# Kernel optimization log

Hardware: AMD Instinct MI355X
Metric: run time of the kernel (lower is better)

Reference implementation:

```python
import jax, jax.numpy as jnp
import numpy as np
import math

B, N, T, H, HEADS, FIN, NL_TR = 4, 256, 16, 128, 4, 2, 5
M = B * N
NEG = -1e9

def _sinusoidal(t, h):
    pos = jnp.arange(t, dtype=jnp.float32)[:, None]
    div = jnp.exp(jnp.arange(0, h, 2, dtype=jnp.float32) * (-math.log(10000.0) / h))
    pe = jnp.zeros((t, h), dtype=jnp.float32)
    pe = pe.at[:, 0::2].set(jnp.sin(pos * div))
    pe = pe.at[:, 1::2].set(jnp.cos(pos * div))
    return pe

def _gat(x, W, a_src, a_dst, b, E, m):
    # x: [T,M,F]; W: [F,heads,H]; E: [T,M,M] bool, E[t,i,j]=edge j->i; m: [T,M] bool
    h = jnp.einsum('tmf,fhd->tmhd', x, W)
    ss = jnp.einsum('tmhd,hd->tmh', h, a_src)  # source score per node
    sd = jnp.einsum('tmhd,hd->tmh', h, a_dst)  # dest score per node
    logits = jax.nn.leaky_relu(sd[:, :, None, :] + ss[:, None, :, :], 0.2)  # [T,i,j,h]
    logits = jnp.where(E[..., None], logits, NEG)
    alpha = jax.nn.softmax(logits, axis=2)  # segment-softmax over incoming edges
    out = jnp.einsum('tijh,tjhd->tihd', alpha, h).mean(axis=2) + b  # concat=False -> head mean + bias
    return jax.nn.relu(out) * m[..., None]

def _ln(x, s, b):
    mu = x.mean(-1, keepdims=True)
    v = ((x - mu) ** 2).mean(-1, keepdims=True)
    return (x - mu) / jnp.sqrt(v + 1e-5) * s + b

def _forward(ego_mask, positions, adjacency, gat1_W, gat1_asrc, gat1_adst, gat1_b, gatW, gat_asrc, gat_adst, gat_b, Wqkv, bqkv, Wo, bo, ln1_s, ln1_b, ln2_s, ln2_b, Wff1, bff1, Wff2, bff2):
    m = jnp.transpose(ego_mask, (1, 0, 2)).reshape(T, M)  # [T, B*N]
    eye = jnp.eye(M, dtype=bool)
    # edge j->i valid iff A[t,j,i]!=0 and both nodes masked; PyG GATConv adds self-loops
    E = ((jnp.swapaxes(adjacency, 1, 2) != 0) & m[:, :, None] & m[:, None, :]) | (eye[None] & m[:, :, None])
    x = _gat(positions, gat1_W, gat1_asrc, gat1_adst, gat1_b, E, m)
    for i in range(5):
        x = _gat(x, gatW[i], gat_asrc[i], gat_adst[i], gat_b[i], E, m)
    x_seq = jnp.transpose(x, (1, 0, 2)) + _sinusoidal(T, H)[None]  # [M, T, H]
    dh = H // HEADS
    scale = 1.0 / math.sqrt(dh)
    for l in range(NL_TR):
        q = (x_seq @ Wqkv[l, 0] + bqkv[l, 0]).reshape(M, T, HEADS, dh)
        k = (x_seq @ Wqkv[l, 1] + bqkv[l, 1]).reshape(M, T, HEADS, dh)
        v = (x_seq @ Wqkv[l, 2] + bqkv[l, 2]).reshape(M, T, HEADS, dh)
        sc = jnp.einsum('bqhd,bkhd->bhqk', q, k) * scale
        a = jax.nn.softmax(sc, axis=-1)
        o = jnp.einsum('bhqk,bkhd->bqhd', a, v).reshape(M, T, H) @ Wo[l] + bo[l]
        x_seq = _ln(x_seq + o, ln1_s[l], ln1_b[l])
        f = jax.nn.relu(x_seq @ Wff1[l] + bff1[l]) @ Wff2[l] + bff2[l]
        x_seq = _ln(x_seq + f, ln2_s[l], ln2_b[l])
    return x_seq.reshape(B, N, T, H)

def setup_inputs() -> dict:
    key = jax.random.key(0)
    ks = jax.random.split(key, 32)
    s = 0.05
    f32 = jnp.float32
    inp = {
        'ego_mask': jax.random.uniform(ks[0], (B, T, N)) < 0.95,
        'positions': jax.random.normal(ks[1], (T, M, FIN), dtype=f32),
        'adjacency': (jax.random.uniform(ks[2], (T, M, M)) < 0.02).astype(f32),
        'gat1_W': jax.random.normal(ks[3], (FIN, HEADS, H), dtype=f32) * s,
        'gat1_asrc': jax.random.normal(ks[4], (HEADS, H), dtype=f32) * s,
        'gat1_adst': jax.random.normal(ks[5], (HEADS, H), dtype=f32) * s,
        'gat1_b': jnp.zeros((H,), dtype=f32),
        'gatW': jax.random.normal(ks[6], (5, H, HEADS, H), dtype=f32) * s,
        'gat_asrc': jax.random.normal(ks[7], (5, HEADS, H), dtype=f32) * s,
        'gat_adst': jax.random.normal(ks[8], (5, HEADS, H), dtype=f32) * s,
        'gat_b': jnp.zeros((5, H), dtype=f32),
        'Wqkv': jax.random.normal(ks[9], (NL_TR, 3, H, H), dtype=f32) * s,
        'bqkv': jnp.zeros((NL_TR, 3, H), dtype=f32),
        'Wo': jax.random.normal(ks[10], (NL_TR, H, H), dtype=f32) * s,
        'bo': jnp.zeros((NL_TR, H), dtype=f32),
        'ln1_s': jnp.ones((NL_TR, H), dtype=f32),
        'ln1_b': jnp.zeros((NL_TR, H), dtype=f32),
        'ln2_s': jnp.ones((NL_TR, H), dtype=f32),
        'ln2_b': jnp.zeros((NL_TR, H), dtype=f32),
        'Wff1': jax.random.normal(ks[11], (NL_TR, H, 4 * H), dtype=f32) * s,
        'bff1': jnp.zeros((NL_TR, 4 * H), dtype=f32),
        'Wff2': jax.random.normal(ks[12], (NL_TR, 4 * H, H), dtype=f32) * s,
        'bff2': jnp.zeros((NL_TR, H), dtype=f32),
    }
    return inp

def reference(ego_mask, positions, adjacency, gat1_W, gat1_asrc, gat1_adst, gat1_b, gatW, gat_asrc, gat_adst, gat_b, Wqkv, bqkv, Wo, bo, ln1_s, ln1_b, ln2_s, ln2_b, Wff1, bff1, Wff2, bff2):
    return _forward(ego_mask, positions, adjacency, gat1_W, gat1_asrc, gat1_adst, gat1_b, gatW, gat_asrc, gat_adst, gat_b, Wqkv, bqkv, Wo, bo, ln1_s, ln1_b, ln2_s, ln2_b, Wff1, bff1, Wff2, bff2)
```

## Files before the change

### kernel.cpp

```cpp
#include <hip/hip_runtime.h>
#include <hip/hip_bf16.h>

#define TT 16
#define MM 1024
#define HDIM 128
#define NHEADS 4
#define NROWS (TT*MM)
#define MAXDEG 64

typedef __bf16 bf16x8 __attribute__((ext_vector_type(8)));
typedef float f32x4 __attribute__((ext_vector_type(4)));

__device__ __forceinline__ unsigned short f2b(float x) {
    unsigned u = __float_as_uint(x);
    u += 0x7fff + ((u >> 16) & 1);
    return (unsigned short)(u >> 16);
}
__device__ __forceinline__ float bu2f(unsigned short u) {
    return __uint_as_float(((unsigned)u) << 16);
}

__global__ __launch_bounds__(256) void k_init(const int* __restrict__ ego,
                                              float* __restrict__ mfl,
                                              int* __restrict__ cnt) {
    int idx = blockIdx.x * 256 + threadIdx.x;
    int t = idx >> 10, i = idx & 1023;
    int b = i >> 8, n = i & 255;
    mfl[idx] = ego[b * (TT * 256) + t * 256 + n] ? 1.f : 0.f;
    cnt[idx] = 0;
}

__global__ __launch_bounds__(256) void k_edges(const float* __restrict__ adj,
                                               const float* __restrict__ mfl,
                                               int* __restrict__ cnt,
                                               int* __restrict__ nbr) {
    int bid = blockIdx.x;
    int t = bid >> 6, jc = bid & 63;
    int tid = threadIdx.x;
    int i0 = tid * 4;
    int rowb = t * MM;
    float mi[4];
#pragma unroll
    for (int r = 0; r < 4; ++r) mi[r] = mfl[rowb + i0 + r];
    __shared__ float ms[16];
    if (tid < 16) ms[tid] = mfl[rowb + jc * 16 + tid];
    __syncthreads();
    const float* at = adj + (size_t)t * MM * MM;
#pragma unroll 4
    for (int jj = 0; jj < 16; ++jj) {
        int j = jc * 16 + jj;
        float4 a = *(const float4*)(at + (size_t)j * MM + i0);
        float mj = ms[jj];
#pragma unroll
        for (int r = 0; r < 4; ++r) {
            int i = i0 + r;
            bool e;
            if (j == i) e = (mi[r] != 0.f);
            else e = ((&a.x)[r] != 0.f) && (mj != 0.f) && (mi[r] != 0.f);
            if (e) {
                int row = rowb + i;
                int pos = atomicAdd(&cnt[row], 1);
                if (pos < MAXDEG) nbr[(size_t)row * MAXDEG + pos] = j;
            }
        }
    }
}

__global__ __launch_bounds__(256) void k_prep(const float* __restrict__ Wqkv,
                                              const float* __restrict__ Wo,
                                              const float* __restrict__ Wff1,
                                              const float* __restrict__ Wff2,
                                              const float* __restrict__ gW,
                                              unsigned short* __restrict__ Wb) {
    int o = blockIdx.x * 256 + threadIdx.x;
    const float* src; int cs;
    if (o < 122880) {
        int l = o / 24576, r = o % 24576;
        if (r < 6144) {
            int nt = r >> 8, rem = r & 255, ks = rem >> 6, lane = rem & 63;
            int mt = nt >> 3, cc = nt & 7;
            int k = ks * 32 + ((lane >> 4) << 3), c = cc * 16 + (lane & 15);
            src = Wqkv + ((size_t)(l * 3 + mt) * 128 + k) * 128 + c; cs = 128;
        } else if (r < 8192) {
            int u = r - 6144, nt = u >> 8, rem = u & 255, ks = rem >> 6, lane = rem & 63;
            int k = ks * 32 + ((lane >> 4) << 3), c = nt * 16 + (lane & 15);
            src = Wo + (size_t)l * 16384 + (size_t)k * 128 + c; cs = 128;
        } else if (r < 16384) {
            int u = r - 8192, nt = u >> 8, rem = u & 255, ks = rem >> 6, lane = rem & 63;
            int k = ks * 32 + ((lane >> 4) << 3), c = nt * 16 + (lane & 15);
            src = Wff1 + (size_t)l * 65536 + (size_t)k * 512 + c; cs = 512;
        } else {
            int u = r - 16384, nt = u >> 10, rem = u & 1023, ks = rem >> 6, lane = rem & 63;
            int k = ks * 32 + ((lane >> 4) << 3), c = nt * 16 + (lane & 15);
            src = Wff2 + (size_t)l * 65536 + (size_t)k * 128 + c; cs = 128;
        }
    } else {
        int u = o - 122880;
        int l = u >> 13, rr = u & 8191;
        int nt = rr >> 8, rem = rr & 255, ks = rem >> 6, lane = rem & 63;
        int k = ks * 32 + ((lane >> 4) << 3), c = nt * 16 + (lane & 15);
        src = gW + (size_t)l * 65536 + (size_t)k * 512 + c; cs = 512;
    }
    unsigned v[4];
#pragma unroll
    for (int j = 0; j < 4; ++j)
        v[j] = (unsigned)f2b(src[(2 * j) * (size_t)cs]) |
               ((unsigned)f2b(src[(2 * j + 1) * (size_t)cs]) << 16);
    *(uint4*)(Wb + (size_t)o * 8) = make_uint4(v[0], v[1], v[2], v[3]);
}

__global__ __launch_bounds__(128) void k_gat1(const float* __restrict__ x,
                                              const float* __restrict__ W,
                                              const float* __restrict__ asrc,
                                              const float* __restrict__ adst,
                                              unsigned short* __restrict__ h16,
                                              float* __restrict__ ss,
                                              float* __restrict__ sd) {
    int bid = blockIdx.x;
    int row = ((bid & 7) << 11) + (bid >> 3);
    int tid = threadIdx.x;
    float x0 = x[row * 2], x1 = x[row * 2 + 1];
    float s4[4], d4[4];
#pragma unroll
    for (int hh = 0; hh < 4; ++hh) {
        int o = hh * 128 + tid;
        float v = x0 * W[o] + x1 * W[512 + o];
        h16[(size_t)row * 512 + o] = f2b(v);
        s4[hh] = v * asrc[o];
        d4[hh] = v * adst[o];
    }
#pragma unroll
    for (int hh = 0; hh < 4; ++hh)
        for (int off = 32; off; off >>= 1) {
            s4[hh] += __shfl_down(s4[hh], off, 64);
            d4[hh] += __shfl_down(d4[hh], off, 64);
        }
    __shared__ float red[2][2][4];
    if ((tid & 63) == 0) {
        int w = tid >> 6;
#pragma unroll
        for (int hh = 0; hh < 4; ++hh) { red[w][0][hh] = s4[hh]; red[w][1][hh] = d4[hh]; }
    }
    __syncthreads();
    if (tid < 4) ss[row * 4 + tid] = red[0][0][tid] + red[1][0][tid];
    else if (tid < 8) sd[row * 4 + tid - 4] = red[0][1][tid - 4] + red[1][1][tid - 4];
}

__global__ __launch_bounds__(256, 2) void k_gat_h(const unsigned short* __restrict__ x16,
                                                  const unsigned short* __restrict__ Wg,
                                                  const float* __restrict__ asrc,
                                                  const float* __restrict__ adst,
                                                  unsigned short* __restrict__ h16,
                                                  float* __restrict__ ss,
                                                  float* __restrict__ sd) {
    __shared__ __align__(16) unsigned short xb[32 * 136];
    int bid = blockIdx.x;
    int row0 = (((bid & 7) << 6) + (bid >> 3)) * 32;
    int tid = threadIdx.x;
#pragma unroll
    for (int q = 0; q < 2; ++q) {
        int u = tid + q * 256;
        int rr = u >> 4, cc = (u & 15) * 8;
        *(uint4*)(xb + rr * 136 + cc) = *(const uint4*)(x16 + (size_t)(row0 + rr) * 128 + cc);
    }
    __syncthreads();
    const int lane = tid & 63, w = tid >> 6;
    const int mrow = lane & 15, quad = lane >> 4;
    float ps[2][4] = {{0,0,0,0},{0,0,0,0}}, pd[2][4] = {{0,0,0,0},{0,0,0,0}};
#pragma unroll
    for (int ib = 0; ib < 4; ++ib) {
        bf16x8 wb[8];
#pragma unroll
        for (int u = 0; u < 2; ++u) {
            int nt = w * 8 + ib * 2 + u;
#pragma unroll
            for (int ks = 0; ks < 4; ++ks)
                wb[u * 4 + ks] = *(const bf16x8*)(Wg + (size_t)((nt * 4 + ks) * 64 + lane) * 8);
        }
#pragma unroll
        for (int rg = 0; rg < 2; ++rg) {
            bf16x8 af[4];
#pragma unroll
            for (int ks = 0; ks < 4; ++ks)
                af[ks] = *(const bf16x8*)(xb + (rg * 16 + mrow) * 136 + ks * 32 + quad * 8);
            f32x4 acc[2];
            acc[0] = (f32x4){0.f, 0.f, 0.f, 0.f};
            acc[1] = (f32x4){0.f, 0.f, 0.f, 0.f};
#pragma unroll
            for (int u = 0; u < 2; ++u)
#pragma unroll
                for (int ks = 0; ks < 4; ++ks)
                    acc[u] = __builtin_amdgcn_mfma_f32_16x16x32_bf16(af[ks], wb[u * 4 + ks], acc[u], 0, 0, 0);
#pragma unroll
            for (int u = 0; u < 2; ++u) {
                int nt = w * 8 + ib * 2 + u, col = nt * 16 + mrow;
                float as_ = asrc[col], ad_ = adst[col];
#pragma unroll
                for (int r = 0; r < 4; ++r) {
                    float v = acc[u][r];
                    h16[(size_t)(row0 + rg * 16 + quad * 4 + r) * 512 + col] = f2b(v);
                    ps[rg][r] += v * as_; pd[rg][r] += v * ad_;
                }
            }
        }
    }
#pragma unroll
    for (int off = 1; off < 16; off <<= 1)
#pragma unroll
        for (int rg = 0; rg < 2; ++rg)
#pragma unroll
            for (int r = 0; r < 4; ++r) {
                ps[rg][r] += __shfl_xor(ps[rg][r], off, 64);
                pd[rg][r] += __shfl_xor(pd[rg][r], off, 64);
            }
    if (mrow == 0) {
#pragma unroll
        for (int rg = 0; rg < 2; ++rg)
#pragma unroll
            for (int r = 0; r < 4; ++r) {
                int row = row0 + rg * 16 + quad * 4 + r;
                ss[row * 4 + w] = ps[rg][r];
                sd[row * 4 + w] = pd[rg][r];
            }
    }
}

__global__ __launch_bounds__(256, 2) void k_agg(const unsigned short* __restrict__ h16,
                                                const float* __restrict__ ss,
                                                const float* __restrict__ sd,
                                                const int* __restrict__ cnt,
                                                const int* __restrict__ nbr,
                                                const float* __restrict__ mfl,
                                                const float* __restrict__ bias,
                                                unsigned short* __restrict__ xo16) {
    __shared__ float alB[4][MAXDEG][4];
    __shared__ int   nbB[4][MAXDEG];
    __shared__ __align__(16) float partB[4][512];
    int bid = blockIdx.x;
    int row0 = (((bid & 7) << 9) + (bid >> 3)) * 4;
    int tid = threadIdx.x;
    const int w = tid >> 6, lane = tid & 63;
    int row = row0 + w, t = row >> 10;
    bool valid = mfl[row] != 0.f;
    int c = 0;
    if (valid) { c = cnt[row]; if (c > MAXDEG) c = MAXDEG; }
    bool act = lane < c;
    int jreg = 0;
    float lg[4];
    if (act) {
        jreg = nbr[(size_t)row * MAXDEG + lane];
        int jr = t * MM + jreg;
#pragma unroll
        for (int hh = 0; hh < 4; ++hh) {
            float v = sd[row * 4 + hh] + ss[jr * 4 + hh];
            lg[hh] = v > 0.f ? v : 0.2f * v;
        }
    } else {
#pragma unroll
        for (int hh = 0; hh < 4; ++hh) lg[hh] = -1e30f;
    }
    float mx[4];
#pragma unroll
    for (int hh = 0; hh < 4; ++hh) mx[hh] = lg[hh];
#pragma unroll
    for (int off = 32; off; off >>= 1)
#pragma unroll
        for (int hh = 0; hh < 4; ++hh) mx[hh] = fmaxf(mx[hh], __shfl_xor(mx[hh], off, 64));
    float ev[4];
#pragma unroll
    for (int hh = 0; hh < 4; ++hh) ev[hh] = act ? __expf(lg[hh] - mx[hh]) : 0.f;
    float sm[4];
#pragma unroll
    for (int hh = 0; hh < 4; ++hh) sm[hh] = ev[hh];
#pragma unroll
    for (int off = 32; off; off >>= 1)
#pragma unroll
        for (int hh = 0; hh < 4; ++hh) sm[hh] += __shfl_xor(sm[hh], off, 64);
    if (act) {
        float4 a4 = make_float4(ev[0] / sm[0], ev[1] / sm[1], ev[2] / sm[2], ev[3] / sm[3]);
        *(float4*)&alB[w][lane][0] = a4;
        nbB[w][lane] = jreg;
    }
    __syncthreads();
    const int head = lane >> 4;
    float acc[8] = {0, 0, 0, 0, 0, 0, 0, 0};
    const unsigned short* hb = h16 + (size_t)t * MM * 512 + lane * 8;
    for (int n = 0; n < c; ++n) {
        int j = nbB[w][n];
        float a = alB[w][n][head];
        uint4 v = *(const uint4*)(hb + (size_t)j * 512);
        acc[0] += a * bu2f((unsigned short)(v.x & 0xffff));
        acc[1] += a * bu2f((unsigned short)(v.x >> 16));
        acc[2] += a * bu2f((unsigned short)(v.y & 0xffff));
        acc[3] += a * bu2f((unsigned short)(v.y >> 16));
        acc[4] += a * bu2f((unsigned short)(v.z & 0xffff));
        acc[5] += a * bu2f((unsigned short)(v.z >> 16));
        acc[6] += a * bu2f((unsigned short)(v.w & 0xffff));
        acc[7] += a * bu2f((unsigned short)(v.w >> 16));
    }
    *(float4*)&partB[w][lane * 8]     = make_float4(acc[0], acc[1], acc[2], acc[3]);
    *(float4*)&partB[w][lane * 8 + 4] = make_float4(acc[4], acc[5], acc[6], acc[7]);
    __syncthreads();
    {
        int d0 = lane * 2;
        unsigned outp = 0;
#pragma unroll
        for (int q = 0; q < 2; ++q) {
            int d = d0 + q;
            float v = 0.f;
            if (valid) {
                v = 0.25f * (partB[w][d] + partB[w][128 + d] + partB[w][256 + d] + partB[w][384 + d])
                    + bias[d];
                v = fmaxf(v, 0.f);
            }
            outp |= ((unsigned)f2b(v)) << (16 * q);
        }
        *(unsigned*)(xo16 + (size_t)row * 128 + d0) = outp;
    }
}

__device__ __forceinline__ void ln512(float* xs, unsigned short* xbB,
                                      const float* s, const float* b) {
    int tid = threadIdx.x, row = tid >> 4, lane = tid & 15;
    float* xr = xs + row * 128;
    float sum = 0.f;
#pragma unroll
    for (int k2 = 0; k2 < 8; ++k2) sum += xr[lane + 16 * k2];
#pragma unroll
    for (int off = 8; off; off >>= 1) sum += __shfl_xor(sum, off, 16);
    float mean = sum * (1.f / 128.f);
    float vs = 0.f;
#pragma unroll
    for (int k2 = 0; k2 < 8; ++k2) { float d = xr[lane + 16 * k2] - mean; vs += d * d; }
#pragma unroll
    for (int off = 8; off; off >>= 1) vs += __shfl_xor(vs, off, 16);
    float rstd = rsqrtf(vs * (1.f / 128.f) + 1e-5f);
#pragma unroll
    for (int k2 = 0; k2 < 8; ++k2) {
        int d = lane + 16 * k2;
        float v = (xr[d] - mean) * rstd * s[d] + b[d];
        xr[d] = v;
        xbB[row * 136 + d] = f2b(v);
    }
    __syncthreads();
}

__global__ __launch_bounds__(512, 2) void k_tf(const unsigned short* __restrict__ xg,
        const unsigned short* __restrict__ Wb,
        const float* __restrict__ bqkv, const float* __restrict__ bo,
        const float* __restrict__ ln1s, const float* __restrict__ ln1b,
        const float* __restrict__ ln2s, const float* __restrict__ ln2b,
        const float* __restrict__ bff1, const float* __restrict__ bff2,
        float* __restrict__ out) {
    __shared__ __align__(16) float smem[16640];
    float* xs  = smem;
    float* sbB = smem + 4096;
    unsigned short* xbB  = (unsigned short*)(smem + 6144);
    unsigned short* qkvB = (unsigned short*)(smem + 8320);
    const int m0 = blockIdx.x * 2, tid = threadIdx.x;
    const int lane = tid & 63, w = tid >> 6;
    const int sid = w >> 2, w4 = w & 3;
    const int mrow = lane & 15, quad = lane >> 4;
    unsigned short* xb16  = xbB + sid * 2176;
    unsigned short* Qb16  = qkvB + sid * 8320;
    unsigned short* Kb16  = Qb16 + 2176;
    unsigned short* Vb16  = Qb16 + 4352;
    unsigned short* hid16 = Qb16;
    float* sb  = sbB + sid * 1024;
    float* xss = xs + sid * 2048;

    for (int idx = tid; idx < 4096; idx += 512) {
        int sq = idx >> 11, t = (idx >> 7) & 15, d = idx & 127, jj = d >> 1;
        float arg = (float)t * expf(-(float)(2 * jj) * (9.210340371976184f / 128.f));
        float pe = (d & 1) ? cosf(arg) : sinf(arg);
        xs[idx] = bu2f(xg[(size_t)t * (MM * HDIM) + (size_t)(m0 + sq) * HDIM + d]) + pe;
    }
    __syncthreads();
    {
        const int crow = tid >> 4, ccb = (tid & 15) * 8;
        const float* xp = xs + crow * 128 + ccb;
        unsigned v[4];
#pragma unroll
        for (int j = 0; j < 4; ++j)
            v[j] = (unsigned)f2b(xp[2 * j]) | ((unsigned)f2b(xp[2 * j + 1]) << 16);
        *(uint4*)(xbB + crow * 136 + ccb) = make_uint4(v[0], v[1], v[2], v[3]);
    }
    __syncthreads();

    for (int l = 0; l < 5; ++l) {
        const unsigned short* Wl = Wb + (size_t)l * 196608;
        {
            bf16x8 af[4];
#pragma unroll
            for (int ks = 0; ks < 4; ++ks)
                af[ks] = *(const bf16x8*)(xb16 + mrow * 136 + ks * 32 + quad * 8);
#pragma unroll
            for (int ib = 0; ib < 3; ++ib) {
                bf16x8 wb[8];
#pragma unroll
                for (int u = 0; u < 2; ++u) {
                    int nt = w4 * 6 + ib * 2 + u;
                    const unsigned short* bp = Wl + (size_t)(nt * 4) * 512 + lane * 8;
#pragma unroll
                    for (int ks = 0; ks < 4; ++ks)
                        wb[u * 4 + ks] = *(const bf16x8*)(bp + ks * 512);
                }
                f32x4 acc[2];
                acc[0] = (f32x4){0.f, 0.f, 0.f, 0.f};
                acc[1] = (f32x4){0.f, 0.f, 0.f, 0.f};
#pragma unroll
                for (int u = 0; u < 2; ++u)
#pragma unroll
                    for (int ks = 0; ks < 4; ++ks)
                        acc[u] = __builtin_amdgcn_mfma_f32_16x16x32_bf16(af[ks], wb[u * 4 + ks], acc[u], 0, 0, 0);
#pragma unroll
                for (int u = 0; u < 2; ++u) {
                    int nt = w4 * 6 + ib * 2 + u, mt = nt >> 3, cc = nt & 7;
                    int col = cc * 16 + mrow;
                    float bb = bqkv[l * 384 + mt * 128 + col];
                    unsigned short* dst = (mt == 0) ? Qb16 : (mt == 1) ? Kb16 : Vb16;
#pragma unroll
                    for (int r = 0; r < 4; ++r)
                        dst[(quad * 4 + r) * 136 + col] = f2b(acc[u][r] + bb);
                }
            }
        }
        __syncthreads();
        {
            int hh = w4, tq = (tid >> 2) & 15, tk0 = (tid & 3) * 4;
            const unsigned short* qp = Qb16 + tq * 136 + hh * 32;
            float a[4] = {0.f, 0.f, 0.f, 0.f};
#pragma unroll
            for (int d4 = 0; d4 < 4; ++d4) {
                uint4 qv = *(const uint4*)(qp + d4 * 8);
                float qf[8];
                qf[0] = bu2f((unsigned short)(qv.x & 0xffff)); qf[1] = bu2f((unsigned short)(qv.x >> 16));
                qf[2] = bu2f((unsigned short)(qv.y & 0xffff)); qf[3] = bu2f((unsigned short)(qv.y >> 16));
                qf[4] = bu2f((unsigned short)(qv.z & 0xffff)); qf[5] = bu2f((unsigned short)(qv.z >> 16));
                qf[6] = bu2f((unsigned short)(qv.w & 0xffff)); qf[7] = bu2f((unsigned short)(qv.w >> 16));
#pragma unroll
                for (int j = 0; j < 4; ++j) {
                    uint4 kv = *(const uint4*)(Kb16 + (tk0 + j) * 136 + hh * 32 + d4 * 8);
                    a[j] += qf[0] * bu2f((unsigned short)(kv.x & 0xffff));
                    a[j] += qf[1] * bu2f((unsigned short)(kv.x >> 16));
                    a[j] += qf[2] * bu2f((unsigned short)(kv.y & 0xffff));
                    a[j] += qf[3] * bu2f((unsigned short)(kv.y >> 16));
                    a[j] += qf[4] * bu2f((unsigned short)(kv.z & 0xffff));
                    a[j] += qf[5] * bu2f((unsigned short)(kv.z >> 16));
                    a[j] += qf[6] * bu2f((unsigned short)(kv.w & 0xffff));
                    a[j] += qf[7] * bu2f((unsigned short)(kv.w >> 16));
                }
            }
#pragma unroll
            for (int j = 0; j < 4; ++j)
                sb[(tk0 + j) * 64 + hh * 16 + tq] = a[j] * 0.17677669529663687f;
        }
        __syncthreads();
        if (tid < 128) {
            float* sbp = sbB + (tid >> 6) * 1024;
            int cc = tid & 63;
            float mx = -1e30f;
#pragma unroll
            for (int u = 0; u < 16; ++u) mx = fmaxf(mx, sbp[u * 64 + cc]);
            float s = 0.f;
#pragma unroll
            for (int u = 0; u < 16; ++u) { float e = __expf(sbp[u * 64 + cc] - mx); sbp[u * 64 + cc] = e; s += e; }
            float inv = 1.f / s;
#pragma unroll
            for (int u = 0; u < 16; ++u) sbp[u * 64 + cc] *= inv;
        }
        __syncthreads();
        {
            int o = tid & 127, r0p = ((tid >> 7) & 1) * 8, hh = o >> 5;
            float accp[8] = {0, 0, 0, 0, 0, 0, 0, 0};
            for (int u = 0; u < 16; ++u) {
                float vv = bu2f(Vb16[u * 136 + o]);
                const float* pp = sb + u * 64 + hh * 16 + r0p;
#pragma unroll
                for (int r = 0; r < 8; ++r) accp[r] += pp[r] * vv;
            }
#pragma unroll
            for (int r = 0; r < 8; ++r)
                xb16[(r0p + r) * 136 + o] = f2b(accp[r]);
        }
        __syncthreads();
        {
            bf16x8 af[4];
#pragma unroll
            for (int ks = 0; ks < 4; ++ks)
                af[ks] = *(const bf16x8*)(xb16 + mrow * 136 + ks * 32 + quad * 8);
            const unsigned short* Ws = Wl + 49152;
            bf16x8 wb[8];
#pragma unroll
            for (int u = 0; u < 2; ++u) {
                int nt = w4 * 2 + u;
#pragma unroll
                for (int ks = 0; ks < 4; ++ks)
                    wb[u * 4 + ks] = *(const bf16x8*)(Ws + (size_t)((nt * 4 + ks) * 64 + lane) * 8);
            }
            f32x4 acc[2];
            acc[0] = (f32x4){0.f, 0.f, 0.f, 0.f};
            acc[1] = (f32x4){0.f, 0.f, 0.f, 0.f};
#pragma unroll
            for (int u = 0; u < 2; ++u)
#pragma unroll
                for (int ks = 0; ks < 4; ++ks)
                    acc[u] = __builtin_amdgcn_mfma_f32_16x16x32_bf16(af[ks], wb[u * 4 + ks], acc[u], 0, 0, 0);
#pragma unroll
            for (int u = 0; u < 2; ++u) {
                int col = (w4 * 2 + u) * 16 + mrow;
                float bb = bo[l * 128 + col];
#pragma unroll
                for (int r = 0; r < 4; ++r)
                    xss[(quad * 4 + r) * 128 + col] += acc[u][r] + bb;
            }
        }
        __syncthreads();
        ln512(xs, xbB, ln1s + l * 128, ln1b + l * 128);
        {
            bf16x8 af[4];
#pragma unroll
            for (int ks = 0; ks < 4; ++ks)
                af[ks] = *(const bf16x8*)(xb16 + mrow * 136 + ks * 32 + quad * 8);
            const unsigned short* Ws = Wl + 65536;
#pragma unroll
            for (int ib = 0; ib < 4; ++ib) {
                bf16x8 wb[8];
#pragma unroll
                for (int u = 0; u < 2; ++u) {
                    int nt = w4 * 8 + ib * 2 + u;
#pragma unroll
                    for (int ks = 0; ks < 4; ++ks)
                        wb[u * 4 + ks] = *(const bf16x8*)(Ws + (size_t)((nt * 4 + ks) * 64 + lane) * 8);
                }
                f32x4 acc[2];
                acc[0] = (f32x4){0.f, 0.f, 0.f, 0.f};
                acc[1] = (f32x4){0.f, 0.f, 0.f, 0.f};
#pragma unroll
                for (int u = 0; u < 2; ++u)
#pragma unroll
                    for (int ks = 0; ks < 4; ++ks)
                        acc[u] = __builtin_amdgcn_mfma_f32_16x16x32_bf16(af[ks], wb[u * 4 + ks], acc[u], 0, 0, 0);
#pragma unroll
                for (int u = 0; u < 2; ++u) {
                    int col = (w4 * 8 + ib * 2 + u) * 16 + mrow;
                    float bb = bff1[l * 512 + col];
#pragma unroll
                    for (int r = 0; r < 4; ++r) {
                        float v = fmaxf(acc[u][r] + bb, 0.f);
                        hid16[(quad * 4 + r) * 520 + col] = f2b(v);
                    }
                }
            }
        }
        __syncthreads();
        {
            f32x4 a0 = (f32x4){0.f, 0.f, 0.f, 0.f};
            f32x4 a1 = (f32x4){0.f, 0.f, 0.f, 0.f};
            const unsigned short* Ws = Wl + 131072;
            int nt0 = w4 * 2, nt1 = w4 * 2 + 1;
#pragma unroll
            for (int kb = 0; kb < 4; ++kb) {
                bf16x8 afb[4], w0[4], w1[4];
#pragma unroll
                for (int kk = 0; kk < 4; ++kk) {
                    int ks = kb * 4 + kk;
                    afb[kk] = *(const bf16x8*)(hid16 + mrow * 520 + ks * 32 + quad * 8);
                    w0[kk] = *(const bf16x8*)(Ws + (size_t)((nt0 * 16 + ks) * 64 + lane) * 8);
                    w1[kk] = *(const bf16x8*)(Ws + (size_t)((nt1 * 16 + ks) * 64 + lane) * 8);
                }
#pragma unroll
                for (int kk = 0; kk < 4; ++kk) {
                    a0 = __builtin_amdgcn_mfma_f32_16x16x32_bf16(afb[kk], w0[kk], a0, 0, 0, 0);
                    a1 = __builtin_amdgcn_mfma_f32_16x16x32_bf16(afb[kk], w1[kk], a1, 0, 0, 0);
                }
            }
            int col0 = nt0 * 16 + mrow, col1 = nt1 * 16 + mrow;
            float bb0 = bff2[l * 128 + col0], bb1 = bff2[l * 128 + col1];
#pragma unroll
            for (int r = 0; r < 4; ++r) {
                xss[(quad * 4 + r) * 128 + col0] += a0[r] + bb0;
                xss[(quad * 4 + r) * 128 + col1] += a1[r] + bb1;
            }
        }
        __syncthreads();
        ln512(xs, xbB, ln2s + l * 128, ln2b + l * 128);
    }
    for (int idx = tid; idx < 4096; idx += 512)
        out[(size_t)m0 * 2048 + idx] = xs[idx];
}

extern "C" void kernel_launch(void* const* d_in, const int* in_sizes, int n_in,
                              void* d_out, int out_size, void* d_ws, size_t ws_size,
                              hipStream_t stream) {
    (void)in_sizes; (void)n_in; (void)out_size; (void)ws_size;
    const int*   ego  = (const int*)d_in[0];
    const float* pos  = (const float*)d_in[1];
    const float* adj  = (const float*)d_in[2];
    const float* g1W  = (const float*)d_in[3];
    const float* g1as = (const float*)d_in[4];
    const float* g1ad = (const float*)d_in[5];
    const float* g1b  = (const float*)d_in[6];
    const float* gW   = (const float*)d_in[7];
    const float* gas  = (const float*)d_in[8];
    const float* gad  = (const float*)d_in[9];
    const float* gb   = (const float*)d_in[10];
    const float* Wqkv = (const float*)d_in[11];
    const float* bqkv = (const float*)d_in[12];
    const float* Wo   = (const float*)d_in[13];
    const float* bo   = (const float*)d_in[14];
    const float* l1s  = (const float*)d_in[15];
    const float* l1b  = (const float*)d_in[16];
    const float* l2s  = (const float*)d_in[17];
    const float* l2b  = (const float*)d_in[18];
    const float* Wff1 = (const float*)d_in[19];
    const float* bff1 = (const float*)d_in[20];
    const float* Wff2 = (const float*)d_in[21];
    const float* bff2 = (const float*)d_in[22];

    unsigned short* x0  = (unsigned short*)d_ws;
    unsigned short* x1  = x0 + 2097152;
    unsigned short* h16 = x1 + 2097152;
    float* ssb = (float*)(h16 + 8388608);
    float* sdb = ssb + 65536;
    float* mfl = sdb + 65536;
    int*   cnt = (int*)(mfl + 16384);
    int*   nbr = cnt + 16384;
    unsigned short* Wb16 = (unsigned short*)(nbr + 1048576);
    unsigned short* Wg16 = Wb16 + 983040;

    k_prep<<<640, 256, 0, stream>>>(Wqkv, Wo, Wff1, Wff2, gW, Wb16);
    k_init<<<64, 256, 0, stream>>>(ego, mfl, cnt);
    k_edges<<<1024, 256, 0, stream>>>(adj, mfl, cnt, nbr);

    k_gat1<<<NROWS, 128, 0, stream>>>(pos, g1W, g1as, g1ad, h16, ssb, sdb);
    k_agg<<<4096, 256, 0, stream>>>(h16, ssb, sdb, cnt, nbr, mfl, g1b, x0);

    unsigned short* xin = x0; unsigned short* xout = x1;
    for (int L = 0; L < 5; ++L) {
        k_gat_h<<<512, 256, 0, stream>>>(xin, Wg16 + (size_t)L * 65536,
                                         gas + L * 512, gad + L * 512, h16, ssb, sdb);
        k_agg<<<4096, 256, 0, stream>>>(h16, ssb, sdb, cnt, nbr, mfl, gb + L * 128, xout);
        unsigned short* tmp = xin; xin = xout; xout = tmp;
    }

    k_tf<<<512, 512, 0, stream>>>(xin, Wb16, bqkv, bo, l1s, l1b, l2s, l2b,
                                  bff1, bff2, (float*)d_out);
}
```

Measured before the change: 525.3 us.

## Halve transformer block threads so each wave reuses weight fragments across both sequences

The fused transformer kernel now runs with 256 threads instead of 512. Each wave handles both sequences of the block, so every weight fragment loaded from global memory feeds MFMAs for two sequences instead of one. This halves redundant weight loads from L2/global. In exchange each thread does twice the attention, softmax-output and layernorm work, with more registers and less wave-level parallelism per block.

```diff
diff --git a/kernel.cpp b/kernel.cpp
--- a/kernel.cpp
+++ b/kernel.cpp
@@ -319,33 +319,38 @@
     }
 }
 
-__device__ __forceinline__ void ln512(float* xs, unsigned short* xbB,
-                                      const float* s, const float* b) {
-    int tid = threadIdx.x, row = tid >> 4, lane = tid & 15;
-    float* xr = xs + row * 128;
-    float sum = 0.f;
-#pragma unroll
-    for (int k2 = 0; k2 < 8; ++k2) sum += xr[lane + 16 * k2];
-#pragma unroll
-    for (int off = 8; off; off >>= 1) sum += __shfl_xor(sum, off, 16);
-    float mean = sum * (1.f / 128.f);
-    float vs = 0.f;
-#pragma unroll
-    for (int k2 = 0; k2 < 8; ++k2) { float d = xr[lane + 16 * k2] - mean; vs += d * d; }
-#pragma unroll
-    for (int off = 8; off; off >>= 1) vs += __shfl_xor(vs, off, 16);
-    float rstd = rsqrtf(vs * (1.f / 128.f) + 1e-5f);
-#pragma unroll
-    for (int k2 = 0; k2 < 8; ++k2) {
-        int d = lane + 16 * k2;
-        float v = (xr[d] - mean) * rstd * s[d] + b[d];
-        xr[d] = v;
-        xbB[row * 136 + d] = f2b(v);
-    }
-    __syncthreads();
-}
-
-__global__ __launch_bounds__(512, 2) void k_tf(const unsigned short* __restrict__ xg,
+__device__ __forceinline__ void ln2x(float* xs, unsigned short* xbB,
+                                     const float* s, const float* b) {
+    int tid = threadIdx.x, lane = tid & 15;
+#pragma unroll
+    for (int half = 0; half < 2; ++half) {
+        int rr = (tid >> 4) + half * 16;
+        float* xr = xs + rr * 128;
+        float sum = 0.f;
+#pragma unroll
+        for (int k2 = 0; k2 < 8; ++k2) sum += xr[lane + 16 * k2];
+#pragma unroll
+        for (int off = 8; off; off >>= 1) sum += __shfl_xor(sum, off, 16);
+        float mean = sum * (1.f / 128.f);
+        float vs = 0.f;
+#pragma unroll
+        for (int k2 = 0; k2 < 8; ++k2) { float d = xr[lane + 16 * k2] - mean; vs += d * d; }
+#pragma unroll
+        for (int off = 8; off; off >>= 1) vs += __shfl_xor(vs, off, 16);
+        float rstd = rsqrtf(vs * (1.f / 128.f) + 1e-5f);
+        unsigned short* xb = xbB + (rr >> 4) * 2176 + (rr & 15) * 136;
+#pragma unroll
+        for (int k2 = 0; k2 < 8; ++k2) {
+            int d = lane + 16 * k2;
+            float v = (xr[d] - mean) * rstd * s[d] + b[d];
+            xr[d] = v;
+            xb[d] = f2b(v);
+        }
+    }
+    __syncthreads();
+}
+
+__global__ __launch_bounds__(256, 2) void k_tf(const unsigned short* __restrict__ xg,
         const unsigned short* __restrict__ Wb,
         const float* __restrict__ bqkv, const float* __restrict__ bo,
         const float* __restrict__ ln1s, const float* __restrict__ ln1b,
@@ -359,101 +364,107 @@
     unsigned short* qkvB = (unsigned short*)(smem + 8320);
     const int m0 = blockIdx.x * 2, tid = threadIdx.x;
     const int lane = tid & 63, w = tid >> 6;
-    const int sid = w >> 2, w4 = w & 3;
     const int mrow = lane & 15, quad = lane >> 4;
-    unsigned short* xb16  = xbB + sid * 2176;
-    unsigned short* Qb16  = qkvB + sid * 8320;
-    unsigned short* Kb16  = Qb16 + 2176;
-    unsigned short* Vb16  = Qb16 + 4352;
-    unsigned short* hid16 = Qb16;
-    float* sb  = sbB + sid * 1024;
-    float* xss = xs + sid * 2048;
-
-    for (int idx = tid; idx < 4096; idx += 512) {
+
+    for (int idx = tid; idx < 4096; idx += 256) {
         int sq = idx >> 11, t = (idx >> 7) & 15, d = idx & 127, jj = d >> 1;
         float arg = (float)t * expf(-(float)(2 * jj) * (9.210340371976184f / 128.f));
         float pe = (d & 1) ? cosf(arg) : sinf(arg);
         xs[idx] = bu2f(xg[(size_t)t * (MM * HDIM) + (size_t)(m0 + sq) * HDIM + d]) + pe;
     }
     __syncthreads();
-    {
-        const int crow = tid >> 4, ccb = (tid & 15) * 8;
-        const float* xp = xs + crow * 128 + ccb;
+#pragma unroll
+    for (int half = 0; half < 2; ++half) {
+        int u = tid + half * 256;
+        int rr = u >> 4, cc = (u & 15) * 8;
+        const float* xp = xs + rr * 128 + cc;
         unsigned v[4];
 #pragma unroll
         for (int j = 0; j < 4; ++j)
             v[j] = (unsigned)f2b(xp[2 * j]) | ((unsigned)f2b(xp[2 * j + 1]) << 16);
-        *(uint4*)(xbB + crow * 136 + ccb) = make_uint4(v[0], v[1], v[2], v[3]);
+        *(uint4*)(xbB + (rr >> 4) * 2176 + (rr & 15) * 136 + cc) = make_uint4(v[0], v[1], v[2], v[3]);
     }
     __syncthreads();
 
     for (int l = 0; l < 5; ++l) {
         const unsigned short* Wl = Wb + (size_t)l * 196608;
         {
-            bf16x8 af[4];
-#pragma unroll
-            for (int ks = 0; ks < 4; ++ks)
-                af[ks] = *(const bf16x8*)(xb16 + mrow * 136 + ks * 32 + quad * 8);
+            bf16x8 af[2][4];
+#pragma unroll
+            for (int sid = 0; sid < 2; ++sid)
+#pragma unroll
+                for (int ks = 0; ks < 4; ++ks)
+                    af[sid][ks] = *(const bf16x8*)(xbB + sid * 2176 + mrow * 136 + ks * 32 + quad * 8);
 #pragma unroll
             for (int ib = 0; ib < 3; ++ib) {
                 bf16x8 wb[8];
 #pragma unroll
                 for (int u = 0; u < 2; ++u) {
-                    int nt = w4 * 6 + ib * 2 + u;
+                    int nt = w * 6 + ib * 2 + u;
                     const unsigned short* bp = Wl + (size_t)(nt * 4) * 512 + lane * 8;
 #pragma unroll
                     for (int ks = 0; ks < 4; ++ks)
                         wb[u * 4 + ks] = *(const bf16x8*)(bp + ks * 512);
                 }
-                f32x4 acc[2];
-                acc[0] = (f32x4){0.f, 0.f, 0.f, 0.f};
-                acc[1] = (f32x4){0.f, 0.f, 0.f, 0.f};
-#pragma unroll
-                for (int u = 0; u < 2; ++u)
-#pragma unroll
-                    for (int ks = 0; ks < 4; ++ks)
-                        acc[u] = __builtin_amdgcn_mfma_f32_16x16x32_bf16(af[ks], wb[u * 4 + ks], acc[u], 0, 0, 0);
-#pragma unroll
-                for (int u = 0; u < 2; ++u) {
-                    int nt = w4 * 6 + ib * 2 + u, mt = nt >> 3, cc = nt & 7;
-                    int col = cc * 16 + mrow;
-                    float bb = bqkv[l * 384 + mt * 128 + col];
-                    unsigned short* dst = (mt == 0) ? Qb16 : (mt == 1) ? Kb16 : Vb16;
-#pragma unroll
-                    for (int r = 0; r < 4; ++r)
-                        dst[(quad * 4 + r) * 136 + col] = f2b(acc[u][r] + bb);
-                }
+                f32x4 acc[2][2];
+#pragma unroll
+                for (int sid = 0; sid < 2; ++sid)
+#pragma unroll
+                    for (int u = 0; u < 2; ++u) acc[sid][u] = (f32x4){0.f, 0.f, 0.f, 0.f};
+#pragma unroll
+                for (int sid = 0; sid < 2; ++sid)
+#pragma unroll
+                    for (int u = 0; u < 2; ++u)
+#pragma unroll
+                        for (int ks = 0; ks < 4; ++ks)
+                            acc[sid][u] = __builtin_amdgcn_mfma_f32_16x16x32_bf16(af[sid][ks], wb[u * 4 + ks], acc[sid][u], 0, 0, 0);
+#pragma unroll
+                for (int sid = 0; sid < 2; ++sid)
+#pragma unroll
+                    for (int u = 0; u < 2; ++u) {
+                        int nt = w * 6 + ib * 2 + u, mt = nt >> 3, cc = nt & 7;
+                        int col = cc * 16 + mrow;
+                        float bb = bqkv[l * 384 + mt * 128 + col];
+                        unsigned short* dst = qkvB + sid * 6528 + mt * 2176;
+#pragma unroll
+                        for (int r = 0; r < 4; ++r)
+                            dst[(quad * 4 + r) * 136 + col] = f2b(acc[sid][u][r] + bb);
+                    }
             }
         }
         __syncthreads();
         {
-            int hh = w4, tq = (tid >> 2) & 15, tk0 = (tid & 3) * 4;
-            const unsigned short* qp = Qb16 + tq * 136 + hh * 32;
-            float a[4] = {0.f, 0.f, 0.f, 0.f};
-#pragma unroll
-            for (int d4 = 0; d4 < 4; ++d4) {
-                uint4 qv = *(const uint4*)(qp + d4 * 8);
-                float qf[8];
-                qf[0] = bu2f((unsigned short)(qv.x & 0xffff)); qf[1] = bu2f((unsigned short)(qv.x >> 16));
-                qf[2] = bu2f((unsigned short)(qv.y & 0xffff)); qf[3] = bu2f((unsigned short)(qv.y >> 16));
-                qf[4] = bu2f((unsigned short)(qv.z & 0xffff)); qf[5] = bu2f((unsigned short)(qv.z >> 16));
-                qf[6] = bu2f((unsigned short)(qv.w & 0xffff)); qf[7] = bu2f((unsigned short)(qv.w >> 16));
-#pragma unroll
-                for (int j = 0; j < 4; ++j) {
-                    uint4 kv = *(const uint4*)(Kb16 + (tk0 + j) * 136 + hh * 32 + d4 * 8);
-                    a[j] += qf[0] * bu2f((unsigned short)(kv.x & 0xffff));
-                    a[j] += qf[1] * bu2f((unsigned short)(kv.x >> 16));
-                    a[j] += qf[2] * bu2f((unsigned short)(kv.y & 0xffff));
-                    a[j] += qf[3] * bu2f((unsigned short)(kv.y >> 16));
-                    a[j] += qf[4] * bu2f((unsigned short)(kv.z & 0xffff));
-                    a[j] += qf[5] * bu2f((unsigned short)(kv.z >> 16));
-                    a[j] += qf[6] * bu2f((unsigned short)(kv.w & 0xffff));
-                    a[j] += qf[7] * bu2f((unsigned short)(kv.w >> 16));
-                }
-            }
-#pragma unroll
-            for (int j = 0; j < 4; ++j)
-                sb[(tk0 + j) * 64 + hh * 16 + tq] = a[j] * 0.17677669529663687f;
+            int hh = tid >> 6, tq = (tid >> 2) & 15, tk0 = (tid & 3) * 4;
+#pragma unroll
+            for (int sid = 0; sid < 2; ++sid) {
+                const unsigned short* qp = qkvB + sid * 6528 + tq * 136 + hh * 32;
+                const unsigned short* kb = qkvB + sid * 6528 + 2176;
+                float a[4] = {0.f, 0.f, 0.f, 0.f};
+#pragma unroll
+                for (int d4 = 0; d4 < 4; ++d4) {
+                    uint4 qv = *(const uint4*)(qp + d4 * 8);
+                    float qf[8];
+                    qf[0] = bu2f((unsigned short)(qv.x & 0xffff)); qf[1] = bu2f((unsigned short)(qv.x >> 16));
+                    qf[2] = bu2f((unsigned short)(qv.y & 0xffff)); qf[3] = bu2f((unsigned short)(qv.y >> 16));
+                    qf[4] = bu2f((unsigned short)(qv.z & 0xffff)); qf[5] = bu2f((unsigned short)(qv.z >> 16));
+                    qf[6] = bu2f((unsigned short)(qv.w & 0xffff)); qf[7] = bu2f((unsigned short)(qv.w >> 16));
+#pragma unroll
+                    for (int j = 0; j < 4; ++j) {
+                        uint4 kv = *(const uint4*)(kb + (tk0 + j) * 136 + hh * 32 + d4 * 8);
+                        a[j] += qf[0] * bu2f((unsigned short)(kv.x & 0xffff));
+                        a[j] += qf[1] * bu2f((unsigned short)(kv.x >> 16));
+                        a[j] += qf[2] * bu2f((unsigned short)(kv.y & 0xffff));
+                        a[j] += qf[3] * bu2f((unsigned short)(kv.y >> 16));
+                        a[j] += qf[4] * bu2f((unsigned short)(kv.z & 0xffff));
+                        a[j] += qf[5] * bu2f((unsigned short)(kv.z >> 16));
+                        a[j] += qf[6] * bu2f((unsigned short)(kv.w & 0xffff));
+                        a[j] += qf[7] * bu2f((unsigned short)(kv.w >> 16));
+                    }
+                }
+#pragma unroll
+                for (int j = 0; j < 4; ++j)
+                    sbB[sid * 1024 + (tk0 + j) * 64 + hh * 16 + tq] = a[j] * 0.17677669529663687f;
+            }
         }
         __syncthreads();
         if (tid < 128) {
@@ -471,122 +482,154 @@
         }
         __syncthreads();
         {
-            int o = tid & 127, r0p = ((tid >> 7) & 1) * 8, hh = o >> 5;
-            float accp[8] = {0, 0, 0, 0, 0, 0, 0, 0};
-            for (int u = 0; u < 16; ++u) {
-                float vv = bu2f(Vb16[u * 136 + o]);
-                const float* pp = sb + u * 64 + hh * 16 + r0p;
-#pragma unroll
-                for (int r = 0; r < 8; ++r) accp[r] += pp[r] * vv;
-            }
-#pragma unroll
-            for (int r = 0; r < 8; ++r)
-                xb16[(r0p + r) * 136 + o] = f2b(accp[r]);
+            int o = tid & 127, r0p = (tid >> 7) * 8, hh = o >> 5;
+#pragma unroll
+            for (int sid = 0; sid < 2; ++sid) {
+                const unsigned short* vb = qkvB + sid * 6528 + 4352;
+                const float* sb = sbB + sid * 1024;
+                float accp[8] = {0, 0, 0, 0, 0, 0, 0, 0};
+                for (int u = 0; u < 16; ++u) {
+                    float vv = bu2f(vb[u * 136 + o]);
+                    const float* pp = sb + u * 64 + hh * 16 + r0p;
+#pragma unroll
+                    for (int r = 0; r < 8; ++r) accp[r] += pp[r] * vv;
+                }
+#pragma unroll
+                for (int r = 0; r < 8; ++r)
+                    xbB[sid * 2176 + (r0p + r) * 136 + o] = f2b(accp[r]);
+            }
         }
         __syncthreads();
         {
-            bf16x8 af[4];
-#pragma unroll
-            for (int ks = 0; ks < 4; ++ks)
-                af[ks] = *(const bf16x8*)(xb16 + mrow * 136 + ks * 32 + quad * 8);
+            bf16x8 af[2][4];
+#pragma unroll
+            for (int sid = 0; sid < 2; ++sid)
+#pragma unroll
+                for (int ks = 0; ks < 4; ++ks)
+                    af[sid][ks] = *(const bf16x8*)(xbB + sid * 2176 + mrow * 136 + ks * 32 + quad * 8);
             const unsigned short* Ws = Wl + 49152;
             bf16x8 wb[8];
 #pragma unroll
             for (int u = 0; u < 2; ++u) {
-                int nt = w4 * 2 + u;
+                int nt = w * 2 + u;
 #pragma unroll
                 for (int ks = 0; ks < 4; ++ks)
                     wb[u * 4 + ks] = *(const bf16x8*)(Ws + (size_t)((nt * 4 + ks) * 64 + lane) * 8);
             }
-            f32x4 acc[2];
-            acc[0] = (f32x4){0.f, 0.f, 0.f, 0.f};
-            acc[1] = (f32x4){0.f, 0.f, 0.f, 0.f};
-#pragma unroll
-            for (int u = 0; u < 2; ++u)
+            f32x4 acc[2][2];
+#pragma unroll
+            for (int sid = 0; sid < 2; ++sid)
+#pragma unroll
+                for (int u = 0; u < 2; ++u) acc[sid][u] = (f32x4){0.f, 0.f, 0.f, 0.f};
+#pragma unroll
+            for (int sid = 0; sid < 2; ++sid)
+#pragma unroll
+                for (int u = 0; u < 2; ++u)
+#pragma unroll
+                    for (int ks = 0; ks < 4; ++ks)
+                        acc[sid][u] = __builtin_amdgcn_mfma_f32_16x16x32_bf16(af[sid][ks], wb[u * 4 + ks], acc[sid][u], 0, 0, 0);
+#pragma unroll
+            for (int sid = 0; sid < 2; ++sid)
+#pragma unroll
+                for (int u = 0; u < 2; ++u) {
+                    int col = (w * 2 + u) * 16 + mrow;
+                    float bb = bo[l * 128 + col];
+#pragma unroll
+                    for (int r = 0; r < 4; ++r)
+                        xs[sid * 2048 + (quad * 4 + r) * 128 + col] += acc[sid][u][r] + bb;
+                }
+        }
+        __syncthreads();
+        ln2x(xs, xbB, ln1s + l * 128, ln1b + l * 128);
+        {
+            bf16x8 af[2][4];
+#pragma unroll
+            for (int sid = 0; sid < 2; ++sid)
 #pragma unroll
                 for (int ks = 0; ks < 4; ++ks)
-                    acc[u] = __builtin_amdgcn_mfma_f32_16x16x32_bf16(af[ks], wb[u * 4 + ks], acc[u], 0, 0, 0);
-#pragma unroll
-            for (int u = 0; u < 2; ++u) {
-                int col = (w4 * 2 + u) * 16 + mrow;
-                float bb = bo[l * 128 + col];
-#pragma unroll
-                for (int r = 0; r < 4; ++r)
-                    xss[(quad * 4 + r) * 128 + col] += acc[u][r] + bb;
-            }
-        }
-        __syncthreads();
-        ln512(xs, xbB, ln1s + l * 128, ln1b + l * 128);
-        {
-            bf16x8 af[4];
-#pragma unroll
-            for (int ks = 0; ks < 4; ++ks)
-                af[ks] = *(const bf16x8*)(xb16 + mrow * 136 + ks * 32 + quad * 8);
+                    af[sid][ks] = *(const bf16x8*)(xbB + sid * 2176 + mrow * 136 + ks * 32 + quad * 8);
             const unsigned short* Ws = Wl + 65536;
 #pragma unroll
             for (int ib = 0; ib < 4; ++ib) {
                 bf16x8 wb[8];
 #pragma unroll
                 for (int u = 0; u < 2; ++u) {
-                    int nt = w4 * 8 + ib * 2 + u;
+                    int nt = w * 8 + ib * 2 + u;
 #pragma unroll
                     for (int ks = 0; ks < 4; ++ks)
                         wb[u * 4 + ks] = *(const bf16x8*)(Ws + (size_t)((nt * 4 + ks) * 64 + lane) * 8);
                 }
-                f32x4 acc[2];
-                acc[0] = (f32x4){0.f, 0.f, 0.f, 0.f};
-                acc[1] = (f32x4){0.f, 0.f, 0.f, 0.f};
-#pragma unroll
-                for (int u = 0; u < 2; ++u)
-#pragma unroll
-                    for (int ks = 0; ks < 4; ++ks)
-                        acc[u] = __builtin_amdgcn_mfma_f32_16x16x32_bf16(af[ks], wb[u * 4 + ks], acc[u], 0, 0, 0);
-#pragma unroll
-                for (int u = 0; u < 2; ++u) {
-                    int col = (w4 * 8 + ib * 2 + u) * 16 + mrow;
-                    float bb = bff1[l * 512 + col];
-#pragma unroll
-                    for (int r = 0; r < 4; ++r) {
-                        float v = fmaxf(acc[u][r] + bb, 0.f);
-                        hid16[(quad * 4 + r) * 520 + col] = f2b(v);
+                f32x4 acc[2][2];
+#pragma unroll
+                for (int sid = 0; sid < 2; ++sid)
+#pragma unroll
+                    for (int u = 0; u < 2; ++u) acc[sid][u] = (f32x4){0.f, 0.f, 0.f, 0.f};
+#pragma unroll
+                for (int sid = 0; sid < 2; ++sid)
+#pragma unroll
+                    for (int u = 0; u < 2; ++u)
+#pragma unroll
+                        for (int ks = 0; ks < 4; ++ks)
+                            acc[sid][u] = __builtin_amdgcn_mfma_f32_16x16x32_bf16(af[sid][ks], wb[u * 4 + ks], acc[sid][u], 0, 0, 0);
+#pragma unroll
+                for (int sid = 0; sid < 2; ++sid)
+#pragma unroll
+                    for (int u = 0; u < 2; ++u) {
+                        int col = (w * 8 + ib * 2 + u) * 16 + mrow;
+                        float bb = bff1[l * 512 + col];
+                        unsigned short* hid16 = qkvB + sid * 8320;
+#pragma unroll
+                        for (int r = 0; r < 4; ++r) {
+                            float v = fmaxf(acc[sid][u][r] + bb, 0.f);
+                            hid16[(quad * 4 + r) * 520 + col] = f2b(v);
+                        }
                     }
-                }
             }
         }
         __syncthreads();
         {
-            f32x4 a0 = (f32x4){0.f, 0.f, 0.f, 0.f};
-            f32x4 a1 = (f32x4){0.f, 0.f, 0.f, 0.f};
+            f32x4 a[2][2];
+#pragma unroll
+            for (int sid = 0; sid < 2; ++sid)
+#pragma unroll
+                for (int u = 0; u < 2; ++u) a[sid][u] = (f32x4){0.f, 0.f, 0.f, 0.f};
             const unsigned short* Ws = Wl + 131072;
-            int nt0 = w4 * 2, nt1 = w4 * 2 + 1;
+            int nt0 = w * 2, nt1 = w * 2 + 1;
 #pragma unroll
             for (int kb = 0; kb < 4; ++kb) {
-                bf16x8 afb[4], w0[4], w1[4];
+                bf16x8 w0[4], w1[4];
 #pragma unroll
                 for (int kk = 0; kk < 4; ++kk) {
                     int ks = kb * 4 + kk;
-                    afb[kk] = *(const bf16x8*)(hid16 + mrow * 520 + ks * 32 + quad * 8);
                     w0[kk] = *(const bf16x8*)(Ws + (size_t)((nt0 * 16 + ks) * 64 + lane) * 8);
                     w1[kk] = *(const bf16x8*)(Ws + (size_t)((nt1 * 16 + ks) * 64 + lane) * 8);
                 }
 #pragma unroll
-                for (int kk = 0; kk < 4; ++kk) {
-                    a0 = __builtin_amdgcn_mfma_f32_16x16x32_bf16(afb[kk], w0[kk], a0, 0, 0, 0);
-                    a1 = __builtin_amdgcn_mfma_f32_16x16x32_bf16(afb[kk], w1[kk], a1, 0, 0, 0);
+                for (int sid = 0; sid < 2; ++sid) {
+                    const unsigned short* hid16 = qkvB + sid * 8320;
+#pragma unroll
+                    for (int kk = 0; kk < 4; ++kk) {
+                        int ks = kb * 4 + kk;
+                        bf16x8 afb = *(const bf16x8*)(hid16 + mrow * 520 + ks * 32 + quad * 8);
+                        a[sid][0] = __builtin_amdgcn_mfma_f32_16x16x32_bf16(afb, w0[kk], a[sid][0], 0, 0, 0);
+                        a[sid][1] = __builtin_amdgcn_mfma_f32_16x16x32_bf16(afb, w1[kk], a[sid][1], 0, 0, 0);
+                    }
                 }
             }
             int col0 = nt0 * 16 + mrow, col1 = nt1 * 16 + mrow;
             float bb0 = bff2[l * 128 + col0], bb1 = bff2[l * 128 + col1];
 #pragma unroll
-            for (int r = 0; r < 4; ++r) {
-                xss[(quad * 4 + r) * 128 + col0] += a0[r] + bb0;
-                xss[(quad * 4 + r) * 128 + col1] += a1[r] + bb1;
-            }
+            for (int sid = 0; sid < 2; ++sid)
+#pragma unroll
+                for (int r = 0; r < 4; ++r) {
+                    xs[sid * 2048 + (quad * 4 + r) * 128 + col0] += a[sid][0][r] + bb0;
+                    xs[sid * 2048 + (quad * 4 + r) * 128 + col1] += a[sid][1][r] + bb1;
+                }
         }
         __syncthreads();
-        ln512(xs, xbB, ln2s + l * 128, ln2b + l * 128);
-    }
-    for (int idx = tid; idx < 4096; idx += 512)
+        ln2x(xs, xbB, ln2s + l * 128, ln2b + l * 128);
+    }
+    for (int idx = tid; idx < 4096; idx += 256)
         out[(size_t)m0 * 2048 + idx] = xs[idx];
 }
 
@@ -644,6 +687,6 @@
         unsigned short* tmp = xin; xin = xout; xout = tmp;
     }
 
-    k_tf<<<512, 512, 0, stream>>>(xin, Wb16, bqkv, bo, l1s, l1b, l2s, l2b,
+    k_tf<<<512, 256, 0, stream>>>(xin, Wb16, bqkv, bo, l1s, l1b, l2s, l2b,
                                   bff1, bff2, (float*)d_out);
 }
```

Result: faster. 491.9 us, median of 3 (-6.3%).
